# Optimization experiments

Measured on AMD Instinct MI355X. Metric: run time of the kernel, lower is better.

Reference implementation:

```python
import jax, jax.numpy as jnp
import numpy as np

B, T, C = 2, 2048, 2048
NH, HS = 16, 128          # heads, head_size = C // NH
NLQ, NLKV = 512, 512      # q / kv latent dims
DHR = 64                  # decoupled rope head dim


def _rope_cos_sin(T, dhr, dtype=jnp.float32):
    inv = 1.0 / (10000.0 ** (np.arange(0, dhr, 2, dtype=np.float32) / dhr))
    ang = np.arange(T, dtype=np.float32)[:, None] * inv[None, :]  # [T, dhr//2]
    return jnp.asarray(np.cos(ang), dtype), jnp.asarray(np.sin(ang), dtype)


def setup_inputs() -> dict:
    key = jax.random.key(0)
    ks = jax.random.split(key, 10)
    s = 0.02
    cos, sin = _rope_cos_sin(T, DHR)
    return {
        "x":     jax.random.normal(ks[0], (B, T, C), jnp.float32),
        "cos":   cos,
        "sin":   sin,
        "W_dq":  s * jax.random.normal(ks[1], (NLQ, C), jnp.float32),
        "W_uq":  s * jax.random.normal(ks[2], (C, NLQ), jnp.float32),
        "W_dkv": s * jax.random.normal(ks[3], (NLKV, C), jnp.float32),
        "W_uk":  s * jax.random.normal(ks[4], (C, NLKV), jnp.float32),
        "W_uv":  s * jax.random.normal(ks[5], (C, NLKV), jnp.float32),
        "W_qr":  s * jax.random.normal(ks[6], (NH * DHR, NLQ), jnp.float32),
        "W_kr":  s * jax.random.normal(ks[7], (DHR, C), jnp.float32),
        "W_o":   s * jax.random.normal(ks[8], (C, C), jnp.float32),
    }


def _apply_rope(x, cos, sin):
    # x: [B, T, H, D]; pairs are interleaved (even=real, odd=imag)
    xr = x.reshape(x.shape[:-1] + (-1, 2))
    re, im = xr[..., 0], xr[..., 1]
    c = cos[None, :, None, :]
    s = sin[None, :, None, :]
    out = jnp.stack([re * c - im * s, re * s + im * c], axis=-1)
    return out.reshape(x.shape)


def reference(x, cos, sin, W_dq, W_uq, W_dkv, W_uk, W_uv, W_qr, W_kr, W_o):
    b, t, c = x.shape
    nh, hs, nlq, nlkv, dhr = NH, HS, NLQ, NLKV, DHR
    scale = 1.0 / np.sqrt(hs + dhr).astype(np.float32)

    # low-rank latents
    c_q = x @ W_dq.T          # [B, T, nlq]
    c_kv = x @ W_dkv.T        # [B, T, nlkv]

    # absorbed matrices (training path)
    # W_uq: [C, nlq] viewed as [nlq, nh, hs]; W_uk: [C, nlkv] viewed as [nh, hs, nlkv]
    k_eff = jnp.einsum('qhd,hdk->hqk', W_uq.reshape(nlq, nh, hs),
                       W_uk.reshape(nh, hs, nlkv))              # [nh, nlq, nlkv]
    v_eff = (W_uv.T @ W_o.T).reshape(nlkv, nh, hs).transpose(1, 0, 2)  # [nh, nlkv, hs]

    # content scores via absorbed low-rank path
    qk = jnp.einsum('btq,hqk->bhtk', c_q, k_eff)                # [B, nh, T, nlkv]
    attn_c = jnp.einsum('bhtk,bsk->bhts', qk, c_kv)             # [B, nh, T, T]

    # decoupled RoPE scores
    c_kr = (x @ W_kr.T)[:, :, None, :]                          # [B, T, 1, dhr]
    k_r = _apply_rope(c_kr, cos, sin)[:, :, 0, :]               # [B, T, dhr]
    c_qr = (c_q @ W_qr.T).reshape(b, t, nh, dhr)
    q_r = _apply_rope(c_qr, cos, sin)                            # [B, T, nh, dhr]
    attn_r = jnp.einsum('bthd,bsd->bhts', q_r, k_r)             # [B, nh, T, T]

    attn = (attn_c + attn_r) * scale
    mask = jnp.tril(jnp.ones((t, t), dtype=bool))
    attn = jnp.where(mask[None, None], attn, -jnp.inf)
    p = jax.nn.softmax(attn, axis=-1)

    ctx = jnp.einsum('bhts,bsk->bhtk', p, c_kv)                 # [B, nh, T, nlkv]
    y = jnp.einsum('bhtk,hkd->bthd', ctx, v_eff).reshape(b, t, c)
    return y
```

## Files before the change

kernel.cpp:

```cpp
#include <hip/hip_runtime.h>
#include <hip/hip_bf16.h>
#include <math.h>

typedef long long ll;
typedef unsigned short ushort_t;
typedef __attribute__((ext_vector_type(8))) __bf16 bf16x8;
typedef __attribute__((ext_vector_type(4))) float f32x4;

__device__ __forceinline__ ushort_t f2bf(float f) {
    __hip_bfloat16 h = __float2bfloat16(f);
    return *reinterpret_cast<ushort_t*>(&h);
}
__device__ __forceinline__ float bf2f(ushort_t u) {
    return __uint_as_float(((unsigned)u) << 16);
}
__device__ __forceinline__ void stage16(const void* g_lane, void* lds_uniform) {
    __builtin_amdgcn_global_load_lds(
        (const __attribute__((address_space(1))) unsigned int*)g_lane,
        (__attribute__((address_space(3))) unsigned int*)lds_uniform, 16, 0, 0);
}

#define DPPMAX(v, ctrl) v = fmaxf(v, __uint_as_float((unsigned)__builtin_amdgcn_update_dpp( \
        0, (int)__float_as_uint(v), (ctrl), 0xF, 0xF, true)))
#define DPPADD(v, ctrl) v = v + __uint_as_float((unsigned)__builtin_amdgcn_update_dpp( \
        0, (int)__float_as_uint(v), (ctrl), 0xF, 0xF, true))
__device__ __forceinline__ float red_max16(float v) {
    DPPMAX(v, 0xB1); DPPMAX(v, 0x4E); DPPMAX(v, 0x141); DPPMAX(v, 0x140); return v;
}
__device__ __forceinline__ float red_sum16(float v) {
    DPPADD(v, 0xB1); DPPADD(v, 0x4E); DPPADD(v, 0x141); DPPADD(v, 0x140); return v;
}

#define TM 128
#define TN 128
#define TK 64

__global__ __launch_bounds__(256)
void gemm_bf16(const ushort_t* __restrict__ Ab, const ushort_t* __restrict__ Bb,
               void* __restrict__ Cb,
               int M, int N, int K,
               int a_rs, int b_rs, int c_rs, int Z2,
               ll a_bs1, ll a_bs2, ll b_bs1, ll b_bs2, ll c_bs1, ll c_bs2,
               int out_f32)
{
    const int m0 = blockIdx.y * TM;
    const int n0 = blockIdx.x * TN;
    const int z1 = blockIdx.z / Z2, z2 = blockIdx.z % Z2;

    const ushort_t* A = Ab + z1 * a_bs1 + z2 * a_bs2;
    const ushort_t* B = Bb + z1 * b_bs1 + z2 * b_bs2;

    __shared__ ushort_t As[2][TM][TK];
    __shared__ ushort_t Bs[2][TN][TK];

    const int tid  = threadIdx.x;
    const int w    = tid >> 6;
    const int l    = tid & 63;
    const int lo16 = l & 15;
    const int quad = l >> 4;
    const int wm0  = (w & 1) * 64;
    const int wn0  = (w >> 1) * 64;

    const int srow  = l >> 3;
    const int sunit = (l & 7) ^ srow;

    f32x4 acc[4][4];
    const f32x4 zero = {0.f, 0.f, 0.f, 0.f};
#pragma unroll
    for (int mi = 0; mi < 4; ++mi)
#pragma unroll
        for (int nj = 0; nj < 4; ++nj) acc[mi][nj] = zero;

    const int nIter = K / TK;

#pragma unroll
    for (int i = 0; i < 4; ++i) {
        const int rr = w * 32 + i * 8;
        stage16(A + (ll)(m0 + rr + srow) * a_rs + sunit * 8, &As[0][rr][0]);
        stage16(B + (ll)(n0 + rr + srow) * b_rs + sunit * 8, &Bs[0][rr][0]);
    }

    int buf = 0;
    for (int it = 0; it < nIter; ++it) {
        __syncthreads();
        if (it + 1 < nIter) {
            const int k0 = (it + 1) * TK;
            const int nb = buf ^ 1;
#pragma unroll
            for (int i = 0; i < 4; ++i) {
                const int rr = w * 32 + i * 8;
                stage16(A + (ll)(m0 + rr + srow) * a_rs + (k0 + sunit * 8), &As[nb][rr][0]);
                stage16(B + (ll)(n0 + rr + srow) * b_rs + (k0 + sunit * 8), &Bs[nb][rr][0]);
            }
        }
#pragma unroll
        for (int h = 0; h < 2; ++h) {
            const int phys = (h * 4 + quad) ^ (lo16 & 7);
            bf16x8 af[4], bfr[4];
#pragma unroll
            for (int mi = 0; mi < 4; ++mi)
                af[mi] = *(const bf16x8*)&As[buf][wm0 + mi * 16 + lo16][phys * 8];
#pragma unroll
            for (int nj = 0; nj < 4; ++nj)
                bfr[nj] = *(const bf16x8*)&Bs[buf][wn0 + nj * 16 + lo16][phys * 8];
#pragma unroll
            for (int mi = 0; mi < 4; ++mi)
#pragma unroll
                for (int nj = 0; nj < 4; ++nj)
                    acc[mi][nj] = __builtin_amdgcn_mfma_f32_16x16x32_bf16(
                        af[mi], bfr[nj], acc[mi][nj], 0, 0, 0);
        }
        buf ^= 1;
    }

    if (out_f32) {
        float* C = (float*)Cb + z1 * c_bs1 + z2 * c_bs2;
#pragma unroll
        for (int mi = 0; mi < 4; ++mi)
#pragma unroll
            for (int r = 0; r < 4; ++r) {
                const ll row = m0 + wm0 + mi * 16 + quad * 4 + r;
                float* cr = C + row * (ll)c_rs + (n0 + wn0 + lo16);
#pragma unroll
                for (int nj = 0; nj < 4; ++nj) cr[nj * 16] = acc[mi][nj][r];
            }
    } else {
        ushort_t* C = (ushort_t*)Cb + z1 * c_bs1 + z2 * c_bs2;
#pragma unroll
        for (int mi = 0; mi < 4; ++mi)
#pragma unroll
            for (int r = 0; r < 4; ++r) {
                const ll row = m0 + wm0 + mi * 16 + quad * 4 + r;
                ushort_t* cr = C + row * (ll)c_rs + (n0 + wn0 + lo16);
#pragma unroll
                for (int nj = 0; nj < 4; ++nj) cr[nj * 16] = f2bf(acc[mi][nj][r]);
            }
    }
}

#define QP_RS 3072
#define XP_RS 1152

__global__ __launch_bounds__(256, 2)
void flash_mla(const ushort_t* __restrict__ QP,
               const ushort_t* __restrict__ WukT,
               const ushort_t* __restrict__ XP,
               const ushort_t* __restrict__ VT,
               float* __restrict__ out,
               float scale)
{
    const int h  = blockIdx.y;
    const int b  = blockIdx.z;

    __shared__ __align__(16) char smem[49152];
    ushort_t* Ks = (ushort_t*)smem;
    ushort_t* Vs = (ushort_t*)(smem + 36864);
    ushort_t* Bw = (ushort_t*)smem;
    ushort_t* Q3 = (ushort_t*)(smem + 16384);

    const int tid  = threadIdx.x;
    const int w    = tid >> 6;
    const int l    = tid & 63;
    const int lo16 = l & 15;
    const int quad = l >> 4;
    char* Pw = smem + 45056 + w * 1024;

#pragma unroll 1
    for (int half = 0; half < 2; ++half) {
        const int qt = half ? (int)blockIdx.x : 31 - (int)blockIdx.x;
        const int t0 = qt * 64;

        __syncthreads();

        bf16x8 qa[18];

#pragma unroll
        for (int i = 0; i < 4; ++i) {
            int p = w * 256 + i * 64 + l;
            int r = p >> 4, u = p & 15, ul = u ^ (r & 15);
            stage16(WukT + ((ll)h * 512 + r) * 128 + ul * 8,
                    (char*)Bw + (ll)(w * 256 + i * 64) * 16);
        }
        bf16x8 ab[4];
#pragma unroll
        for (int kd = 0; kd < 4; ++kd)
            ab[kd] = *(const bf16x8*)(QP + (ll)(b * 2048 + t0 + 16 * w + lo16) * QP_RS +
                                      h * 128 + kd * 32 + quad * 8);
        __syncthreads();

        for (int kc = 0; kc < 8; ++kc) {
#pragma unroll
            for (int nt = 0; nt < 4; ++nt) {
                f32x4 c = {0.f, 0.f, 0.f, 0.f};
#pragma unroll
                for (int kd = 0; kd < 4; ++kd) {
                    bf16x8 bb = *(const bf16x8*)(Bw + (nt * 16 + lo16) * 128 +
                                                 (((kd * 4 + quad) ^ lo16) & 15) * 8);
                    c = __builtin_amdgcn_mfma_f32_16x16x32_bf16(ab[kd], bb, c, 0, 0, 0);
                }
#pragma unroll
                for (int r = 0; r < 4; ++r)
                    Q3[(w * 16 + quad * 4 + r) * 72 + nt * 16 + lo16] = f2bf(c[r]);
            }
#pragma unroll
            for (int kd2 = 0; kd2 < 2; ++kd2)
                qa[kc * 2 + kd2] = *(const bf16x8*)(Q3 + (w * 16 + lo16) * 72 + kd2 * 32 + quad * 8);

            if (kc < 7) {
                __syncthreads();
#pragma unroll
                for (int i = 0; i < 4; ++i) {
                    int p = w * 256 + i * 64 + l;
                    int r = p >> 4, u = p & 15, ul = u ^ (r & 15);
                    stage16(WukT + ((ll)h * 512 + (kc + 1) * 64 + r) * 128 + ul * 8,
                            (char*)Bw + (ll)(w * 256 + i * 64) * 16);
                }
                __syncthreads();
            }
        }
#pragma unroll
        for (int kt = 16; kt < 18; ++kt)
            qa[kt] = *(const bf16x8*)(QP + (ll)(b * 2048 + t0 + 16 * w + lo16) * QP_RS +
                                      2048 + h * 64 + (kt - 16) * 32 + quad * 8);

        f32x4 oacc[8];
        const f32x4 zero = {0.f, 0.f, 0.f, 0.f};
#pragma unroll
        for (int dt = 0; dt < 8; ++dt) oacc[dt] = zero;
        float mrow[4], lrow[4];
#pragma unroll
        for (int r = 0; r < 4; ++r) { mrow[r] = -3.0e38f; lrow[r] = 0.f; }

        const int nst = 2 * qt + 2;
        for (int st = 0; st < nst; ++st) {
            const int s0 = st * 32;
            __syncthreads();
#pragma unroll
            for (int i = 0; i < 9; ++i) {
                int p = i * 64 + l;
                int r = 8 * w + p / 72, u = p % 72, ul = u ^ (r & 7);
                stage16(XP + (ll)(b * 2048 + s0 + r) * XP_RS + 512 + ul * 8,
                        (char*)Ks + (ll)(w * 576 + i * 64) * 16);
            }
#pragma unroll
            for (int i = 0; i < 2; ++i) {
                int p = w * 128 + i * 64 + l;
                int r = p >> 2, u = p & 3, ul = u ^ (r & 3);
                stage16(VT + ((ll)(b * 16 + h) * 128 + r) * 2048 + s0 + ul * 8,
                        (char*)Vs + (ll)(w * 128 + i * 64) * 16);
            }
            __syncthreads();

            f32x4 sc[2];
            sc[0] = zero; sc[1] = zero;
            __builtin_amdgcn_s_setprio(1);
#pragma unroll
            for (int kt = 0; kt < 18; ++kt)
#pragma unroll
                for (int nt = 0; nt < 2; ++nt) {
                    int phys = (kt * 4 + quad) ^ (lo16 & 7);
                    bf16x8 kb = *(const bf16x8*)(Ks + (nt * 16 + lo16) * 576 + phys * 8);
                    sc[nt] = __builtin_amdgcn_mfma_f32_16x16x32_bf16(qa[kt], kb, sc[nt], 0, 0, 0);
                }
            __builtin_amdgcn_s_setprio(0);

            const int rbase = 16 * w + quad * 4;
#pragma unroll
            for (int nt = 0; nt < 2; ++nt)
#pragma unroll
                for (int r = 0; r < 4; ++r) sc[nt][r] *= scale;
            if (st >= 2 * qt) {
#pragma unroll
                for (int nt = 0; nt < 2; ++nt)
#pragma unroll
                    for (int r = 0; r < 4; ++r)
                        if ((s0 + nt * 16 + lo16) > (t0 + rbase + r))
                            sc[nt][r] = -INFINITY;
            }

            float alpha[4];
#pragma unroll
            for (int r = 0; r < 4; ++r) {
                float tm = red_max16(fmaxf(sc[0][r], sc[1][r]));
                float mnew = fmaxf(mrow[r], tm);
                alpha[r] = __expf(mrow[r] - mnew);
                mrow[r] = mnew;
                sc[0][r] = __expf(sc[0][r] - mnew);
                sc[1][r] = __expf(sc[1][r] - mnew);
                float rs = red_sum16(sc[0][r] + sc[1][r]);
                lrow[r] = lrow[r] * alpha[r] + rs;
            }
#pragma unroll
            for (int dt = 0; dt < 8; ++dt)
#pragma unroll
                for (int r = 0; r < 4; ++r) oacc[dt][r] *= alpha[r];

#pragma unroll
            for (int nt = 0; nt < 2; ++nt)
#pragma unroll
                for (int r = 0; r < 4; ++r) {
                    int row = quad * 4 + r;
                    int col = nt * 16 + lo16;
                    *(ushort_t*)(Pw + row * 64 + (((col >> 3) ^ (row & 3)) << 4) + (col & 7) * 2)
                        = f2bf(sc[nt][r]);
                }
            bf16x8 pf = *(const bf16x8*)(Pw + lo16 * 64 + (quad ^ (lo16 & 3)) * 16);

            __builtin_amdgcn_s_setprio(1);
#pragma unroll
            for (int dt = 0; dt < 8; ++dt) {
                int phys = quad ^ (lo16 & 3);
                bf16x8 vb = *(const bf16x8*)(Vs + (dt * 16 + lo16) * 32 + phys * 8);
                oacc[dt] = __builtin_amdgcn_mfma_f32_16x16x32_bf16(pf, vb, oacc[dt], 0, 0, 0);
            }
            __builtin_amdgcn_s_setprio(0);
        }

#pragma unroll
        for (int r = 0; r < 4; ++r) {
            const float inv = 1.0f / lrow[r];
            const ll row = (ll)(b * 2048 + t0 + 16 * w + quad * 4 + r);
#pragma unroll
            for (int dt = 0; dt < 8; ++dt)
                out[row * 2048 + h * 128 + dt * 16 + lo16] = oacc[dt][r] * inv;
        }
    }
}

__global__ void cvt_f32_bf16(const float* __restrict__ in, ushort_t* __restrict__ out, ll n4)
{
    ll i = (ll)blockIdx.x * 256 + threadIdx.x;
    if (i >= n4) return;
    float4 v = *(const float4*)(in + i * 4);
    ushort4 u;
    u.x = f2bf(v.x); u.y = f2bf(v.y); u.z = f2bf(v.z); u.w = f2bf(v.w);
    *(ushort4*)(out + i * 4) = u;
}

__global__ void build_wb1(const float* __restrict__ Wdq, const float* __restrict__ Wdkv,
                          const float* __restrict__ Wkr, ushort_t* __restrict__ out)
{
    ll i4 = ((ll)blockIdx.x * 256 + threadIdx.x) * 4;
    if (i4 >= (ll)1152 * 2048) return;
    int row = (int)(i4 >> 11);
    int col = (int)(i4 & 2047);
    float4 v = make_float4(0.f, 0.f, 0.f, 0.f);
    if (row < 512)       v = *(const float4*)(Wdq + (ll)row * 2048 + col);
    else if (row < 1024) v = *(const float4*)(Wdkv + (ll)(row - 512) * 2048 + col);
    else if (row < 1088) v = *(const float4*)(Wkr + (ll)(row - 1024) * 2048 + col);
    ushort4 u;
    u.x = f2bf(v.x); u.y = f2bf(v.y); u.z = f2bf(v.z); u.w = f2bf(v.w);
    *(ushort4*)(out + i4) = u;
}

__global__ void transpose_f32_bf16(const float* __restrict__ in, ushort_t* __restrict__ out,
                                   int R, int C, ll in_bs, ll out_bs)
{
    __shared__ float tile[32][33];
    const float* I = in + (ll)blockIdx.z * in_bs;
    ushort_t*    O = out + (ll)blockIdx.z * out_bs;
    int r0 = blockIdx.y * 32, c0 = blockIdx.x * 32;
    int tx = threadIdx.x & 31, ty = threadIdx.x >> 5;
#pragma unroll
    for (int i = 0; i < 4; ++i)
        tile[ty + i * 8][tx] = I[(ll)(r0 + ty + i * 8) * C + (c0 + tx)];
    __syncthreads();
#pragma unroll
    for (int i = 0; i < 4; ++i)
        O[(ll)(c0 + ty + i * 8) * R + (r0 + tx)] = f2bf(tile[tx][ty + i * 8]);
}

__global__ void rope_kr(ushort_t* __restrict__ XP, const float* __restrict__ cb,
                        const float* __restrict__ sb)
{
    int idx = blockIdx.x * 256 + threadIdx.x;
    if (idx >= 2 * 2048 * 32) return;
    int j = idx & 31, t = (idx >> 5) & 2047, b = idx >> 16;
    float c = cb[t * 32 + j], s = sb[t * 32 + j];
    ushort_t* p = XP + ((ll)(b * 2048 + t)) * 1152 + 1024 + 2 * j;
    float re = bf2f(p[0]), im = bf2f(p[1]);
    p[0] = f2bf(re * c - im * s);
    p[1] = f2bf(re * s + im * c);
}

__global__ void rope_qr_ip(ushort_t* __restrict__ QP, const float* __restrict__ cb,
                           const float* __restrict__ sb)
{
    int idx = blockIdx.x * 256 + threadIdx.x;
    if (idx >= 4096 * 512) return;
    int pj = idx & 511, h = pj >> 5, j = pj & 31;
    int row = idx >> 9;
    int t = row & 2047;
    float c = cb[t * 32 + j], s = sb[t * 32 + j];
    ll base = (ll)row * 3072 + 2048 + h * 64 + 2 * j;
    float re = bf2f(QP[base]), im = bf2f(QP[base + 1]);
    QP[base]     = f2bf(re * c - im * s);
    QP[base + 1] = f2bf(re * s + im * c);
}

static inline void gemmb(hipStream_t st, const ushort_t* A, const ushort_t* B, void* C,
                         int M, int N, int K, int a_rs, int b_rs, int c_rs,
                         int nb, int Z2,
                         ll a_bs1, ll a_bs2, ll b_bs1, ll b_bs2, ll c_bs1, ll c_bs2,
                         int of32)
{
    dim3 g(N / TN, M / TM, nb);
    gemm_bf16<<<g, 256, 0, st>>>(A, B, C, M, N, K, a_rs, b_rs, c_rs, Z2,
                                 a_bs1, a_bs2, b_bs1, b_bs2, c_bs1, c_bs2, of32);
}

extern "C" void kernel_launch(void* const* d_in, const int* in_sizes, int n_in,
                              void* d_out, int out_size, void* d_ws, size_t ws_size,
                              hipStream_t stream)
{
    const float* x     = (const float*)d_in[0];
    const float* cosb  = (const float*)d_in[1];
    const float* sinb  = (const float*)d_in[2];
    const float* W_dq  = (const float*)d_in[3];
    const float* W_uq  = (const float*)d_in[4];
    const float* W_dkv = (const float*)d_in[5];
    const float* W_uk  = (const float*)d_in[6];
    const float* W_uv  = (const float*)d_in[7];
    const float* W_qr  = (const float*)d_in[8];
    const float* W_kr  = (const float*)d_in[9];
    const float* W_o   = (const float*)d_in[10];
    float* out = (float*)d_out;

    const float scale = 0.07216878364870323f;

    char* base = (char*)d_ws;
    ushort_t* WB1     = (ushort_t*)(base + 0);
    ushort_t* WukT_b  = (ushort_t*)(base + 4718592);
    ushort_t* WuvT_b  = (ushort_t*)(base + 6815744);
    ushort_t* WB2     = (ushort_t*)(base + 8912896);
    ushort_t* veffT_b = (ushort_t*)(base + 12058624);
    ushort_t* Wo_b    = (ushort_t*)(base + 14155776);
    ushort_t* xb      = (ushort_t*)(base + 22544384);
    ushort_t* XP      = (ushort_t*)(base + 39321600);
    ushort_t* VT_all  = (ushort_t*)(base + 48758784);
    ushort_t* QP      = (ushort_t*)(base + 65536000);

    cvt_f32_bf16<<<8192, 256, 0, stream>>>(x, xb, 2097152);
    cvt_f32_bf16<<<4096, 256, 0, stream>>>(W_o, Wo_b, 1048576);
    build_wb1<<<2304, 256, 0, stream>>>(W_dq, W_dkv, W_kr, WB1);
    transpose_f32_bf16<<<dim3(16, 4, 16), 256, 0, stream>>>(W_uk, WukT_b, 128, 512, 65536, 65536);
    transpose_f32_bf16<<<dim3(16, 64, 1), 256, 0, stream>>>(W_uv, WuvT_b, 2048, 512, 0, 0);
    transpose_f32_bf16<<<dim3(64, 16, 1), 256, 0, stream>>>(W_uq, WB2, 512, 2048, 0, 0);
    cvt_f32_bf16<<<512, 256, 0, stream>>>(W_qr, WB2 + (ll)2048 * 512, 131072);

    gemmb(stream, Wo_b, WuvT_b, veffT_b, 128, 512, 2048, 2048, 2048, 512,
          16, 16, 0, 262144, 0, 0, 0, 65536, 0);

    gemmb(stream, xb, WB1, XP, 4096, 1152, 2048, 2048, 2048, 1152,
          1, 1, 0, 0, 0, 0, 0, 0, 0);
    rope_kr<<<512, 256, 0, stream>>>(XP, cosb, sinb);

    gemmb(stream, veffT_b, XP + 512, VT_all, 128, 2048, 512, 512, 1152, 2048,
          32, 16, 0, 65536, (ll)2048 * 1152, 0, (ll)16 * 262144, 262144, 0);

    gemmb(stream, XP, WB2, QP, 4096, 3072, 512, 1152, 512, 3072,
          1, 1, 0, 0, 0, 0, 0, 0, 0);
    rope_qr_ip<<<8192, 256, 0, stream>>>(QP, cosb, sinb);

    flash_mla<<<dim3(16, 16, 2), 256, 0, stream>>>(QP, WukT_b, XP, VT_all, out, scale);

    (void)in_sizes; (void)n_in; (void)out_size; (void)ws_size;
}
```

Baseline: 456.1 us.

## Process two query tiles per 512-thread block sharing K/V staging

The flash kernel now runs 8 waves per block, split into two groups that each own an adjacent 64-row query tile. The K and V chunks for each step are staged into LDS once and used by both tiles. Staging work is spread across the waves: six load K and two load V, which halves K/V global traffic and staging per query. In exchange, waves whose causal range has ended skip compute but still hit the barriers, so group 0 sits idle for its last steps. The tighter launch bound also raises register pressure, which could cause spills.

```diff
diff --git a/kernel.cpp b/kernel.cpp
--- a/kernel.cpp
+++ b/kernel.cpp
@@ -141,7 +141,7 @@
 #define QP_RS 3072
 #define XP_RS 1152
 
-__global__ __launch_bounds__(256, 2)
+__global__ __launch_bounds__(512, 4)
 void flash_mla(const ushort_t* __restrict__ QP,
                const ushort_t* __restrict__ WukT,
                const ushort_t* __restrict__ XP,
@@ -152,7 +152,7 @@
     const int h  = blockIdx.y;
     const int b  = blockIdx.z;
 
-    __shared__ __align__(16) char smem[49152];
+    __shared__ __align__(16) char smem[53248];
     ushort_t* Ks = (ushort_t*)smem;
     ushort_t* Vs = (ushort_t*)(smem + 36864);
     ushort_t* Bw = (ushort_t*)smem;
@@ -160,31 +160,36 @@
 
     const int tid  = threadIdx.x;
     const int w    = tid >> 6;
+    const int g    = w >> 2;
+    const int wl   = w & 3;
     const int l    = tid & 63;
     const int lo16 = l & 15;
     const int quad = l >> 4;
     char* Pw = smem + 45056 + w * 1024;
 
 #pragma unroll 1
-    for (int half = 0; half < 2; ++half) {
-        const int qt = half ? (int)blockIdx.x : 31 - (int)blockIdx.x;
+    for (int task = 0; task < 2; ++task) {
+        const int jj = task ? (int)blockIdx.x : 15 - (int)blockIdx.x;
+        const int qt = 2 * jj + g;
         const int t0 = qt * 64;
+        const int nstBlk = 4 * jj + 4;
+        const int myLast = 2 * qt + (wl >> 1);
 
         __syncthreads();
 
         bf16x8 qa[18];
 
 #pragma unroll
-        for (int i = 0; i < 4; ++i) {
-            int p = w * 256 + i * 64 + l;
+        for (int i = 0; i < 2; ++i) {
+            int p = w * 128 + i * 64 + l;
             int r = p >> 4, u = p & 15, ul = u ^ (r & 15);
             stage16(WukT + ((ll)h * 512 + r) * 128 + ul * 8,
-                    (char*)Bw + (ll)(w * 256 + i * 64) * 16);
+                    (char*)Bw + (ll)(w * 128 + i * 64) * 16);
         }
         bf16x8 ab[4];
 #pragma unroll
         for (int kd = 0; kd < 4; ++kd)
-            ab[kd] = *(const bf16x8*)(QP + (ll)(b * 2048 + t0 + 16 * w + lo16) * QP_RS +
+            ab[kd] = *(const bf16x8*)(QP + (ll)(b * 2048 + t0 + 16 * wl + lo16) * QP_RS +
                                       h * 128 + kd * 32 + quad * 8);
         __syncthreads();
 
@@ -209,18 +214,18 @@
             if (kc < 7) {
                 __syncthreads();
 #pragma unroll
-                for (int i = 0; i < 4; ++i) {
-                    int p = w * 256 + i * 64 + l;
+                for (int i = 0; i < 2; ++i) {
+                    int p = w * 128 + i * 64 + l;
                     int r = p >> 4, u = p & 15, ul = u ^ (r & 15);
                     stage16(WukT + ((ll)h * 512 + (kc + 1) * 64 + r) * 128 + ul * 8,
-                            (char*)Bw + (ll)(w * 256 + i * 64) * 16);
+                            (char*)Bw + (ll)(w * 128 + i * 64) * 16);
                 }
                 __syncthreads();
             }
         }
 #pragma unroll
         for (int kt = 16; kt < 18; ++kt)
-            qa[kt] = *(const bf16x8*)(QP + (ll)(b * 2048 + t0 + 16 * w + lo16) * QP_RS +
+            qa[kt] = *(const bf16x8*)(QP + (ll)(b * 2048 + t0 + 16 * wl + lo16) * QP_RS +
                                       2048 + h * 64 + (kt - 16) * 32 + quad * 8);
 
         f32x4 oacc[8];
@@ -231,25 +236,29 @@
 #pragma unroll
         for (int r = 0; r < 4; ++r) { mrow[r] = -3.0e38f; lrow[r] = 0.f; }
 
-        const int nst = 2 * qt + 2;
-        for (int st = 0; st < nst; ++st) {
+        for (int st = 0; st < nstBlk; ++st) {
             const int s0 = st * 32;
             __syncthreads();
-#pragma unroll
-            for (int i = 0; i < 9; ++i) {
-                int p = i * 64 + l;
-                int r = 8 * w + p / 72, u = p % 72, ul = u ^ (r & 7);
-                stage16(XP + (ll)(b * 2048 + s0 + r) * XP_RS + 512 + ul * 8,
-                        (char*)Ks + (ll)(w * 576 + i * 64) * 16);
-            }
-#pragma unroll
-            for (int i = 0; i < 2; ++i) {
-                int p = w * 128 + i * 64 + l;
-                int r = p >> 2, u = p & 3, ul = u ^ (r & 3);
-                stage16(VT + ((ll)(b * 16 + h) * 128 + r) * 2048 + s0 + ul * 8,
-                        (char*)Vs + (ll)(w * 128 + i * 64) * 16);
+            if (w < 6) {
+#pragma unroll
+                for (int i = 0; i < 6; ++i) {
+                    int p = w * 384 + i * 64 + l;
+                    int r = p / 72, u = p % 72, ul = u ^ (r & 7);
+                    stage16(XP + (ll)(b * 2048 + s0 + r) * XP_RS + 512 + ul * 8,
+                            (char*)Ks + (ll)(w * 384 + i * 64) * 16);
+                }
+            } else {
+#pragma unroll
+                for (int i = 0; i < 4; ++i) {
+                    int p = (w - 6) * 256 + i * 64 + l;
+                    int r = p >> 2, u = p & 3, ul = u ^ (r & 3);
+                    stage16(VT + ((ll)(b * 16 + h) * 128 + r) * 2048 + s0 + ul * 8,
+                            (char*)Vs + (ll)((w - 6) * 256 + i * 64) * 16);
+                }
             }
             __syncthreads();
+
+            if (st > myLast) continue;
 
             f32x4 sc[2];
             sc[0] = zero; sc[1] = zero;
@@ -264,7 +273,7 @@
                 }
             __builtin_amdgcn_s_setprio(0);
 
-            const int rbase = 16 * w + quad * 4;
+            const int rbase = 16 * wl + quad * 4;
 #pragma unroll
             for (int nt = 0; nt < 2; ++nt)
 #pragma unroll
@@ -319,7 +328,7 @@
 #pragma unroll
         for (int r = 0; r < 4; ++r) {
             const float inv = 1.0f / lrow[r];
-            const ll row = (ll)(b * 2048 + t0 + 16 * w + quad * 4 + r);
+            const ll row = (ll)(b * 2048 + t0 + 16 * wl + quad * 4 + r);
 #pragma unroll
             for (int dt = 0; dt < 8; ++dt)
                 out[row * 2048 + h * 128 + dt * 16 + lo16] = oacc[dt][r] * inv;
@@ -462,7 +471,7 @@
           1, 1, 0, 0, 0, 0, 0, 0, 0);
     rope_qr_ip<<<8192, 256, 0, stream>>>(QP, cosb, sinb);
 
-    flash_mla<<<dim3(16, 16, 2), 256, 0, stream>>>(QP, WukT_b, XP, VT_all, out, scale);
+    flash_mla<<<dim3(16, 16, 2), 512, 0, stream>>>(QP, WukT_b, XP, VT_all, out, scale);
 
     (void)in_sizes; (void)n_in; (void)out_size; (void)ws_size;
 }
```

Measured after the change: 1.257 ms. 176% more time.
